# Performance work log

Hardware: AMD Instinct MI355X
Metric: run time of the kernel (lower is better)

The kernel has to match this reference:

```python
import jax, jax.numpy as jnp
import numpy as np
from jax import lax

B, C, H, W = 2048, 3, 64, 64
NUM_NODES = 20
N = B * NUM_NODES


def _edges():
    # fully-connected (no self loop) 20-node graph, replicated per batch element
    i, j = np.meshgrid(np.arange(NUM_NODES), np.arange(NUM_NODES), indexing='ij')
    m = i != j
    src, dst = i[m], j[m]  # 380 edges per graph
    off = (np.arange(B) * NUM_NODES)[:, None]
    rows = (src[None] + off).reshape(-1)
    cols = (dst[None] + off).reshape(-1)
    return jnp.asarray(np.stack([rows, cols]), dtype=jnp.int32)  # [2, B*380]


def setup_inputs() -> dict:
    key = jax.random.key(0)
    ks = jax.random.split(key, 8)
    return dict(
        im=jax.random.uniform(ks[0], (B, C, H, W), jnp.float32),
        x=jax.random.normal(ks[1], (N, 2), jnp.float32),
        edge_index=_edges(),
        conv1_w=jax.random.normal(ks[2], (10, 3, 11, 11), jnp.float32) * 0.05,
        conv2_w=jax.random.normal(ks[3], (16, 10, 5, 5), jnp.float32) * 0.05,
        conv2_b=jnp.zeros((16,), jnp.float32),
        lin_w=jax.random.normal(ks[4], (2, 64), jnp.float32) * 0.1,
        lin_b=jnp.zeros((2,), jnp.float32),
        g1_w=jax.random.normal(ks[5], (8, 4), jnp.float32) * 0.3,
        g1_b=jnp.zeros((8,), jnp.float32),
        g2_w=jax.random.normal(ks[6], (1, 8), jnp.float32) * 0.3,
        g2_b=jnp.zeros((1,), jnp.float32),
    )


def _maxpool(h, k, s):
    return lax.reduce_window(h, -jnp.inf, lax.max, (1, 1, k, k), (1, 1, s, s), 'VALID')


def _gcn(x, edge_index, Wt, b, improved, aggr):
    # PyG GCNConv: linear (no bias) -> gcn_norm with self-loops -> scatter aggr -> +bias
    x = x @ Wt.T
    n = x.shape[0]
    fill = 2.0 if improved else 1.0  # improved adds self-loop weight 2
    loop = jnp.arange(n, dtype=edge_index.dtype)
    row = jnp.concatenate([edge_index[0], loop])  # source (flow=source_to_target)
    col = jnp.concatenate([edge_index[1], loop])  # target
    ew = jnp.concatenate([jnp.ones(edge_index.shape[1], x.dtype), jnp.full((n,), fill, x.dtype)])
    deg = jax.ops.segment_sum(ew, col, num_segments=n)
    dis = jnp.where(deg > 0, lax.rsqrt(jnp.maximum(deg, 1e-12)), 0.0)
    norm = dis[row] * ew * dis[col]
    msg = norm[:, None] * x[row]  # gather + weight
    if aggr == 'mean':
        s = jax.ops.segment_sum(msg, col, num_segments=n)
        cnt = jax.ops.segment_sum(jnp.ones_like(norm), col, num_segments=n)
        out = s / jnp.maximum(cnt, 1.0)[:, None]
    else:  # max
        out = jax.ops.segment_max(msg, col, num_segments=n)
        out = jnp.where(jnp.isfinite(out), out, 0.0)
    return out + b


def reference(im, x, edge_index, conv1_w, conv2_w, conv2_b, lin_w, lin_b, g1_w, g1_b, g2_w, g2_b):
    dn = ('NCHW', 'OIHW', 'NCHW')
    h = lax.conv_general_dilated(im, conv1_w, (4, 4), [(2, 2), (2, 2)], dimension_numbers=dn)
    h = jax.nn.leaky_relu(h)          # slope 0.01, matches nn.LeakyReLU default
    h = _maxpool(h, 3, 2)             # [B,10,7,7]
    h = lax.conv_general_dilated(h, conv2_w, (2, 2), [(2, 2), (2, 2)], dimension_numbers=dn)
    h = h + conv2_b[None, :, None, None]
    h = jax.nn.leaky_relu(h)
    h = _maxpool(h, 2, 2)             # [B,16,2,2]
    h = h.reshape(-1, 64)
    img_feat = jax.nn.sigmoid(h @ lin_w.T + lin_b)  # [B,2]
    xin = jnp.concatenate([x, jnp.repeat(img_feat, NUM_NODES, axis=0)], axis=1)  # [N,4]
    h1 = jax.nn.leaky_relu(_gcn(xin, edge_index, g1_w, g1_b, False, 'mean'))
    h2 = _gcn(h1, edge_index, g2_w, g2_b, True, 'max')  # [N,1]
    out = jax.nn.softmax(h2.reshape(B, NUM_NODES), axis=1)
    return out, img_feat
```

## Files before the change

kernel.cpp:

```cpp
#include <hip/hip_runtime.h>
#include <math.h>


#define PLW 72
#define PLANE_SH (PLW * 68)
#define OUT1_OFF 9792
#define SMEM_BYTES (OUT1_OFF + 2250 * 4)

typedef __attribute__((ext_vector_type(8))) short bf16x8;
typedef __attribute__((ext_vector_type(4))) float f32x4;

__device__ inline unsigned short f2bf(float f) {
    unsigned u = __float_as_uint(f);
    u += 0x7fff + ((u >> 16) & 1);
    return (unsigned short)(u >> 16);
}

__global__ void reorder_weights(const float* __restrict__ w1,
                                const float* __restrict__ w2,
                                unsigned char* __restrict__ ws) {
    unsigned short* bN = (unsigned short*)ws;
    unsigned short* bS = (unsigned short*)(ws + 33792);
    float* w2t = (float*)(ws + 67584);
    const int id = blockIdx.x * 256 + threadIdx.x;
    for (int e = id; e < 16896; e += 4096) {
        int j = e & 7, lane = (e >> 3) & 63, s = e >> 9;
        int n = lane & 15, q = lane >> 4, slot = q * 8 + j;
        int c = s / 11, ky = s - c * 11;
        unsigned short vN = 0, vS = 0;
        if (n < 10) {
            const float* wr = w1 + n * 363 + c * 121 + ky * 11;
            if (slot < 11) vN = f2bf(wr[slot]);
            int kxS = slot - 4;
            if (kxS >= 0 && kxS < 11) vS = f2bf(wr[kxS]);
        }
        bN[e] = vN;
        bS[e] = vS;
    }
    for (int i = id; i < 4000; i += 4096) {
        int k = i & 15, tap = i >> 4;
        w2t[i] = w2[k * 250 + tap];
    }
}

__global__ __launch_bounds__(256) void cnn_mfma(
        const float* __restrict__ im,
        const unsigned char* __restrict__ wsb,
        const float* __restrict__ conv2_b,
        const float* __restrict__ lin_w,
        const float* __restrict__ lin_b,
        float* __restrict__ out) {
    __shared__ __align__(16) unsigned char smem[SMEM_BYTES];
    unsigned short* plane = (unsigned short*)smem;
    float* out1 = (float*)(smem + OUT1_OFF);
    const int b = blockIdx.x, t = threadIdx.x;
    const int lane = t & 63, wid = t >> 6;
    const int n = lane & 15, q = lane >> 4;

    if (t < 20) out[b * 20 + t] = 0.05f;

    for (int i = t; i < PLANE_SH / 4; i += 256)
        ((unsigned long long*)plane)[i] = 0ull;

    const bool even_cls = (wid < 2);
    const int nt = (wid == 3) ? 3 : 4;
    const int t0 = (wid & 1) * 4;
    const unsigned short* bfr =
        (const unsigned short*)(wsb + (even_cls ? 0 : 33792));

    int ebase[4];
#pragma unroll
    for (int tl = 0; tl < 4; ++tl) {
        int Tl = t0 + ((tl < nt) ? tl : 0);
        int i = Tl * 16 + n;
        int oy, cb;
        if (even_cls) {
            oy = min(i >> 3, 14);
            cb = (i & 7) << 3;
        } else {
            int oyu = i / 7, rem = i - oyu * 7;
            oy = min(oyu, 14);
            cb = rem << 3;
        }
        ebase[tl] = 288 * oy + cb + (q << 3);
    }

    f32x4 acc[4];
#pragma unroll
    for (int i = 0; i < 4; ++i) acc[i] = (f32x4)(0.0f);

    for (int c = 0; c < 3; ++c) {
        __syncthreads();
        const float4* imc = (const float4*)(im + ((size_t)(b * 3 + c)) * 4096);
#pragma unroll
        for (int jj = 0; jj < 4; ++jj) {
            int ii = t + jj * 256;
            float4 v = imc[ii];
            int y = ii >> 4, x4 = (ii & 15) << 2;
            int e = (y + 2) * PLW + x4 + 2;
            *(ushort2*)(&plane[e])     = make_ushort2(f2bf(v.x), f2bf(v.y));
            *(ushort2*)(&plane[e + 2]) = make_ushort2(f2bf(v.z), f2bf(v.w));
        }
        __syncthreads();
        const unsigned short* bsl = bfr + (c * 11) * 512 + lane * 8;
#pragma unroll 1
        for (int ky = 0; ky < 11; ++ky) {
            bf16x8 bf = *(const bf16x8*)(bsl + ky * 512);
            const int ro = ky * PLW;
#pragma unroll
            for (int tl = 0; tl < 4; ++tl) {
                if (tl < nt) {
                    bf16x8 a = *(const bf16x8*)(&plane[ebase[tl] + ro]);
                    acc[tl] = __builtin_amdgcn_mfma_f32_16x16x32_bf16(
                        a, bf, acc[tl], 0, 0, 0);
                }
            }
        }
    }

#pragma unroll
    for (int tl = 0; tl < 4; ++tl) {
        if (tl < nt) {
            int Tl = t0 + tl;
#pragma unroll
            for (int r = 0; r < 4; ++r) {
                int i = Tl * 16 + (q << 2) + r;
                float v = acc[tl][r];
                v = v > 0.0f ? v : 0.01f * v;
                if (n < 10) {
                    if (even_cls) {
                        if (i < 120) out1[n * 225 + (i >> 3) * 15 + ((i & 7) << 1)] = v;
                    } else {
                        if (i < 105) {
                            int oyu = i / 7;
                            out1[n * 225 + oyu * 15 + (i - oyu * 7) * 2 + 1] = v;
                        }
                    }
                }
            }
        }
    }
    __syncthreads();
    float* p1p = (float*)smem;
    for (int i = t; i < 1210; i += 256) p1p[i] = 0.0f;
    __syncthreads();
    for (int i = t; i < 490; i += 256) {
        int c2 = i / 49, r = (i % 49) / 7, col = i % 7;
        const float* o1 = &out1[c2 * 225 + (2 * r) * 15 + 2 * col];
        float m = o1[0];
        m = fmaxf(m, o1[1]);  m = fmaxf(m, o1[2]);
        m = fmaxf(m, o1[15]); m = fmaxf(m, o1[16]); m = fmaxf(m, o1[17]);
        m = fmaxf(m, o1[30]); m = fmaxf(m, o1[31]); m = fmaxf(m, o1[32]);
        p1p[c2 * 121 + (r + 2) * 11 + (col + 2)] = m;
    }
    __syncthreads();
    float* out2 = (float*)(smem + 4864);
    float* hbuf = (float*)(smem + 6144);
    {
        const float* w2t = (const float*)(wsb + 67584);
        const int k = t & 15, pix = t >> 4;
        const int o2y = pix >> 2, o2x = pix & 3;
        float a2 = 0.0f;
#pragma unroll 1
        for (int c2 = 0; c2 < 10; ++c2) {
#pragma unroll
            for (int ky = 0; ky < 5; ++ky) {
#pragma unroll
                for (int kx = 0; kx < 5; ++kx) {
                    float v = p1p[c2 * 121 + (o2y * 2 + ky) * 11 + o2x * 2 + kx];
                    a2 = fmaf(v, w2t[(c2 * 25 + ky * 5 + kx) * 16 + k], a2);
                }
            }
        }
        a2 += conv2_b[k];
        a2 = a2 > 0.0f ? a2 : 0.01f * a2;
        out2[k * 16 + pix] = a2;
    }
    __syncthreads();
    if (t < 64) {
        int k = t >> 2, qy = (t >> 1) & 1, qx = t & 1;
        const float* o2 = &out2[k * 16 + (2 * qy) * 4 + 2 * qx];
        hbuf[t] = fmaxf(fmaxf(o2[0], o2[1]), fmaxf(o2[4], o2[5]));
    }
    __syncthreads();
    if (t < 128) {
        int o = t >> 6, l = t & 63;
        float p = hbuf[l] * lin_w[o * 64 + l];
#pragma unroll
        for (int m = 32; m >= 1; m >>= 1) p += __shfl_xor(p, m);
        if (l == 0)
            out[40960 + b * 2 + o] = 1.0f / (1.0f + expf(-(p + lin_b[o])));
    }
}

__global__ __launch_bounds__(256) void cnn_fallback(
        const float* __restrict__ im, const float* __restrict__ w1,
        const float* __restrict__ w2, const float* __restrict__ conv2_b,
        const float* __restrict__ lin_w, const float* __restrict__ lin_b,
        float* __restrict__ out) {
    __shared__ __align__(16) float bufA[68 * 68];
    const int b = blockIdx.x, t = threadIdx.x;
    if (t < 20) out[b * 20 + t] = 0.05f;
    for (int i = t; i < 68 * 68; i += 256) bufA[i] = 0.0f;
    float acc[10];
#pragma unroll
    for (int i = 0; i < 10; ++i) acc[i] = 0.0f;
    const int oy = min(t / 15, 14), ox = t % 15;
    for (int c = 0; c < 3; ++c) {
        __syncthreads();
        const float4* imc = (const float4*)(im + ((size_t)(b * 3 + c)) * 4096);
        for (int i = t; i < 1024; i += 256) {
            float4 v = imc[i];
            int y = i >> 4, x4 = (i & 15) << 2;
            float* dst = &bufA[(y + 2) * 68 + x4 + 2];
            dst[0] = v.x; dst[1] = v.y; dst[2] = v.z; dst[3] = v.w;
        }
        __syncthreads();
#pragma unroll 1
        for (int ky = 0; ky < 11; ++ky) {
            const float* row = &bufA[(oy * 4 + ky) * 68 + ox * 4];
            float4 r0 = *(const float4*)(row);
            float4 r1 = *(const float4*)(row + 4);
            float4 r2 = *(const float4*)(row + 8);
            float in[12] = {r0.x, r0.y, r0.z, r0.w, r1.x, r1.y, r1.z, r1.w,
                            r2.x, r2.y, r2.z, r2.w};
#pragma unroll
            for (int kx = 0; kx < 11; ++kx) {
                float v = in[kx];
#pragma unroll
                for (int oc = 0; oc < 10; ++oc)
                    acc[oc] = fmaf(v, w1[oc * 363 + c * 121 + ky * 11 + kx], acc[oc]);
            }
        }
    }
    __syncthreads();
    if (t < 225) {
#pragma unroll
        for (int oc = 0; oc < 10; ++oc) {
            float v = acc[oc];
            bufA[oc * 225 + t] = v > 0.0f ? v : 0.01f * v;
        }
    }
    float* p1p = bufA + 3100;
    for (int i = t; i < 1210; i += 256) p1p[i] = 0.0f;
    __syncthreads();
    for (int i = t; i < 490; i += 256) {
        int c2 = i / 49, r = (i % 49) / 7, col = i % 7;
        const float* o1 = &bufA[c2 * 225 + (2 * r) * 15 + 2 * col];
        float m = o1[0];
        m = fmaxf(m, o1[1]);  m = fmaxf(m, o1[2]);
        m = fmaxf(m, o1[15]); m = fmaxf(m, o1[16]); m = fmaxf(m, o1[17]);
        m = fmaxf(m, o1[30]); m = fmaxf(m, o1[31]); m = fmaxf(m, o1[32]);
        p1p[c2 * 121 + (r + 2) * 11 + (col + 2)] = m;
    }
    __syncthreads();
    float* out2 = bufA;
    float* hbuf = bufA + 256;
    {
        const int k = t & 15, pix = t >> 4;
        const int o2y = pix >> 2, o2x = pix & 3;
        float a2 = 0.0f;
#pragma unroll 1
        for (int c2 = 0; c2 < 10; ++c2)
#pragma unroll
            for (int ky = 0; ky < 5; ++ky)
#pragma unroll
                for (int kx = 0; kx < 5; ++kx) {
                    float v = p1p[c2 * 121 + (o2y * 2 + ky) * 11 + o2x * 2 + kx];
                    a2 = fmaf(v, w2[k * 250 + c2 * 25 + ky * 5 + kx], a2);
                }
        a2 += conv2_b[k];
        a2 = a2 > 0.0f ? a2 : 0.01f * a2;
        __syncthreads();
        out2[k * 16 + pix] = a2;
    }
    __syncthreads();
    if (t < 64) {
        int k = t >> 2, qy = (t >> 1) & 1, qx = t & 1;
        const float* o2 = &out2[k * 16 + (2 * qy) * 4 + 2 * qx];
        hbuf[t] = fmaxf(fmaxf(o2[0], o2[1]), fmaxf(o2[4], o2[5]));
    }
    __syncthreads();
    if (t < 128) {
        int o = t >> 6, l = t & 63;
        float p = hbuf[l] * lin_w[o * 64 + l];
#pragma unroll
        for (int m = 32; m >= 1; m >>= 1) p += __shfl_xor(p, m);
        if (l == 0)
            out[40960 + b * 2 + o] = 1.0f / (1.0f + expf(-(p + lin_b[o])));
    }
}

extern "C" void kernel_launch(void* const* d_in, const int* in_sizes, int n_in,
                              void* d_out, int out_size, void* d_ws, size_t ws_size,
                              hipStream_t stream) {
    const float* im = (const float*)d_in[0];
    const float* w1 = (const float*)d_in[3];
    const float* w2 = (const float*)d_in[4];
    const float* b2 = (const float*)d_in[5];
    const float* lw = (const float*)d_in[6];
    const float* lb = (const float*)d_in[7];
    float* out = (float*)d_out;

    if (ws_size >= 83584) {
        reorder_weights<<<16, 256, 0, stream>>>(w1, w2, (unsigned char*)d_ws);
        cnn_mfma<<<2048, 256, 0, stream>>>(im, (const unsigned char*)d_ws,
                                           b2, lw, lb, out);
    } else {
        cnn_fallback<<<2048, 256, 0, stream>>>(im, w1, w2, b2, lw, lb, out);
    }
}
```

Before: 200.0 us.

## Pack two kernel rows per MFMA K-slice and split conv2 channels across waves

The conv1 MFMA loop now packs two kernel rows (ky pairs) into each 32-wide K slice instead of one padded 11-tap row. That cuts the MFMAs per channel from 11 to 6 and shrinks the reordered weight buffers. Conv2 is restructured so each wave handles a subset of input channels with float4 weight loads and 4 output channels per thread, followed by a shared-memory reduction across waves. Image conversion to bf16 uses the packed HIP intrinsic, and a barrier moves ahead of the conv1 epilogue because the out1/p1p regions may alias.

```diff
diff --git a/kernel.cpp b/kernel.cpp
--- a/kernel.cpp
+++ b/kernel.cpp
@@ -1,4 +1,5 @@
 #include <hip/hip_runtime.h>
+#include <hip/hip_bf16.h>
 #include <math.h>
 
 
@@ -20,18 +21,20 @@
                                 const float* __restrict__ w2,
                                 unsigned char* __restrict__ ws) {
     unsigned short* bN = (unsigned short*)ws;
-    unsigned short* bS = (unsigned short*)(ws + 33792);
-    float* w2t = (float*)(ws + 67584);
+    unsigned short* bS = (unsigned short*)(ws + 18432);
+    float* w2t = (float*)(ws + 36864);
     const int id = blockIdx.x * 256 + threadIdx.x;
-    for (int e = id; e < 16896; e += 4096) {
+    for (int e = id; e < 9216; e += 4096) {
         int j = e & 7, lane = (e >> 3) & 63, s = e >> 9;
-        int n = lane & 15, q = lane >> 4, slot = q * 8 + j;
-        int c = s / 11, ky = s - c * 11;
+        int n = lane & 15, q = lane >> 4;
+        int c = s / 6, kyp = s - c * 6;
+        int k = q * 8 + j;
+        int ky = 2 * kyp + (k >> 4);
+        int kxN = k & 15, kxS = (k & 15) - 4;
         unsigned short vN = 0, vS = 0;
-        if (n < 10) {
+        if (n < 10 && ky < 11) {
             const float* wr = w1 + n * 363 + c * 121 + ky * 11;
-            if (slot < 11) vN = f2bf(wr[slot]);
-            int kxS = slot - 4;
+            if (kxN < 11) vN = f2bf(wr[kxN]);
             if (kxS >= 0 && kxS < 11) vS = f2bf(wr[kxS]);
         }
         bN[e] = vN;
@@ -52,6 +55,7 @@
         float* __restrict__ out) {
     __shared__ __align__(16) unsigned char smem[SMEM_BYTES];
     unsigned short* plane = (unsigned short*)smem;
+    float* smemf = (float*)smem;
     float* out1 = (float*)(smem + OUT1_OFF);
     const int b = blockIdx.x, t = threadIdx.x;
     const int lane = t & 63, wid = t >> 6;
@@ -66,8 +70,9 @@
     const int nt = (wid == 3) ? 3 : 4;
     const int t0 = (wid & 1) * 4;
     const unsigned short* bfr =
-        (const unsigned short*)(wsb + (even_cls ? 0 : 33792));
-
+        (const unsigned short*)(wsb + (even_cls ? 0 : 18432));
+
+    const int lofs = (q >> 1) * 72 + (q & 1) * 8;
     int ebase[4];
 #pragma unroll
     for (int tl = 0; tl < 4; ++tl) {
@@ -82,7 +87,7 @@
             oy = min(oyu, 14);
             cb = rem << 3;
         }
-        ebase[tl] = 288 * oy + cb + (q << 3);
+        ebase[tl] = 288 * oy + cb + lofs;
     }
 
     f32x4 acc[4];
@@ -98,15 +103,17 @@
             float4 v = imc[ii];
             int y = ii >> 4, x4 = (ii & 15) << 2;
             int e = (y + 2) * PLW + x4 + 2;
-            *(ushort2*)(&plane[e])     = make_ushort2(f2bf(v.x), f2bf(v.y));
-            *(ushort2*)(&plane[e + 2]) = make_ushort2(f2bf(v.z), f2bf(v.w));
-        }
-        __syncthreads();
-        const unsigned short* bsl = bfr + (c * 11) * 512 + lane * 8;
+            *(__hip_bfloat162*)(&plane[e]) =
+                __float22bfloat162_rn(make_float2(v.x, v.y));
+            *(__hip_bfloat162*)(&plane[e + 2]) =
+                __float22bfloat162_rn(make_float2(v.z, v.w));
+        }
+        __syncthreads();
+        const unsigned short* bsl = bfr + c * 3072 + lane * 8;
 #pragma unroll 1
-        for (int ky = 0; ky < 11; ++ky) {
-            bf16x8 bf = *(const bf16x8*)(bsl + ky * 512);
-            const int ro = ky * PLW;
+        for (int kyp = 0; kyp < 6; ++kyp) {
+            bf16x8 bf = *(const bf16x8*)(bsl + kyp * 512);
+            const int ro = kyp * 144;
 #pragma unroll
             for (int tl = 0; tl < 4; ++tl) {
                 if (tl < nt) {
@@ -118,6 +125,7 @@
         }
     }
 
+    __syncthreads();
 #pragma unroll
     for (int tl = 0; tl < 4; ++tl) {
         if (tl < nt) {
@@ -140,8 +148,7 @@
             }
         }
     }
-    __syncthreads();
-    float* p1p = (float*)smem;
+    float* p1p = smemf;
     for (int i = t; i < 1210; i += 256) p1p[i] = 0.0f;
     __syncthreads();
     for (int i = t; i < 490; i += 256) {
@@ -154,27 +161,38 @@
         p1p[c2 * 121 + (r + 2) * 11 + (col + 2)] = m;
     }
     __syncthreads();
-    float* out2 = (float*)(smem + 4864);
-    float* hbuf = (float*)(smem + 6144);
     {
-        const float* w2t = (const float*)(wsb + 67584);
-        const int k = t & 15, pix = t >> 4;
-        const int o2y = pix >> 2, o2x = pix & 3;
-        float a2 = 0.0f;
+        const float* w2t = (const float*)(wsb + 36864);
+        const int pix2 = lane >> 2, kg = lane & 3;
+        const int o2y = pix2 >> 2, o2x = pix2 & 3;
+        const int c2s = (wid * 10) >> 2, c2e = ((wid + 1) * 10) >> 2;
+        float ax = 0.f, ay = 0.f, az = 0.f, aw = 0.f;
 #pragma unroll 1
-        for (int c2 = 0; c2 < 10; ++c2) {
+        for (int c2 = c2s; c2 < c2e; ++c2) {
 #pragma unroll
             for (int ky = 0; ky < 5; ++ky) {
 #pragma unroll
                 for (int kx = 0; kx < 5; ++kx) {
                     float v = p1p[c2 * 121 + (o2y * 2 + ky) * 11 + o2x * 2 + kx];
-                    a2 = fmaf(v, w2t[(c2 * 25 + ky * 5 + kx) * 16 + k], a2);
+                    float4 w = *(const float4*)(w2t + (c2 * 25 + ky * 5 + kx) * 16 + kg * 4);
+                    ax = fmaf(v, w.x, ax); ay = fmaf(v, w.y, ay);
+                    az = fmaf(v, w.z, az); aw = fmaf(v, w.w, aw);
                 }
             }
         }
-        a2 += conv2_b[k];
-        a2 = a2 > 0.0f ? a2 : 0.01f * a2;
-        out2[k * 16 + pix] = a2;
+        *(float4*)(&smemf[1216 + wid * 256 + pix2 * 16 + kg * 4]) =
+            make_float4(ax, ay, az, aw);
+    }
+    __syncthreads();
+    float* out2 = smemf + 2240;
+    float* hbuf = smemf + 2496;
+    {
+        const int k = t & 15, pix = t >> 4;
+        float s = smemf[1216 + pix * 16 + k] + smemf[1472 + pix * 16 + k] +
+                  smemf[1728 + pix * 16 + k] + smemf[1984 + pix * 16 + k];
+        s += conv2_b[k];
+        s = s > 0.0f ? s : 0.01f * s;
+        out2[k * 16 + pix] = s;
     }
     __syncthreads();
     if (t < 64) {
@@ -302,7 +320,7 @@
     const float* lb = (const float*)d_in[7];
     float* out = (float*)d_out;
 
-    if (ws_size >= 83584) {
+    if (ws_size >= 52864) {
         reorder_weights<<<16, 256, 0, stream>>>(w1, w2, (unsigned char*)d_ws);
         cnn_mfma<<<2048, 256, 0, stream>>>(im, (const unsigned char*)d_ws,
                                            b2, lw, lb, out);
```

After: 191.1 us. -4.4%, faster.
